# Optimization experiments

Hardware: AMD Instinct MI355X
Metric: run time of the kernel (lower is better)

## Reference

```python
import jax, jax.numpy as jnp
import numpy as np

B, C_IN, C_OUT, H, K = 256, 64, 64, 1855, 6


def setup_inputs() -> dict:
    key = jax.random.key(0)
    k1, k2, k3, k4 = jax.random.split(key, 4)
    x = jax.random.normal(k1, (B, C_IN, H), dtype=jnp.float32)
    # hex-grid neighbor table; -1 marks missing neighbors (camera boundary).
    neighbors = jax.random.randint(k2, (H, K), 0, H, dtype=jnp.int32)
    # row 0 fully valid is not required -- module uses row 0 to compute total_valid.
    mask = jax.random.uniform(k3, (H, K)) < 0.1
    neighbors = jnp.where(mask, -1, neighbors)
    weight_center = jax.random.normal(k4, (C_OUT, C_IN), dtype=jnp.float32) / np.sqrt(C_IN)
    weight_neighbors = jax.random.normal(jax.random.fold_in(key, 5), (C_OUT, C_IN, K), dtype=jnp.float32) / np.sqrt(C_IN * K)
    bias = jnp.zeros((C_OUT,), dtype=jnp.float32)
    return {"x": x, "neighbors": neighbors, "weight_center": weight_center,
            "weight_neighbors": weight_neighbors, "bias": bias}


def reference(x, neighbors, weight_center, weight_neighbors, bias):
    # x: [B, C_in, H] -> [B, H, C_in]
    xt = jnp.swapaxes(x, 1, 2)
    # center contribution: [B, H, C_out]
    center = jnp.einsum('bhc,oc->bho', xt, weight_center)
    valid = neighbors >= 0                      # [H, K]
    idx = jnp.where(valid, neighbors, 0)        # safe gather indices
    nf = xt[:, idx]                             # [B, H, K, C_in] gathered neighbors
    nf = nf * valid[None, :, :, None].astype(xt.dtype)
    neighbor_contrib = jnp.einsum('bhkc,ock->bho', nf, weight_neighbors)
    # module divides by (#valid neighbors of hexagon 0) + 1
    total_valid = (valid[0].sum() + 1).astype(xt.dtype)
    out = (center + neighbor_contrib) / total_valid + bias
    return jnp.swapaxes(out, 1, 2)              # [B, C_out, H]
```

## Files before the change

### kernel.cpp

```cpp
#include <hip/hip_runtime.h>
#include <hip/hip_bf16.h>

#define B_    256
#define CIN   64
#define COUT  64
#define H_    1855
#define K_    6
#define NSTEP 14
#define HT    64
#define NHT   29

#define HT2   32
#define TPB   58
#define NTILE (TPB * B_)
#define TPBLK 8
#define NBLK  (NTILE / TPBLK)
#define CPX2  (NBLK / 8)

typedef __bf16 bf16x8 __attribute__((ext_vector_type(8)));
typedef float  f32x4  __attribute__((ext_vector_type(4)));

typedef __attribute__((address_space(3))) unsigned int       lds_u32;
typedef const __attribute__((address_space(1))) unsigned int glb_u32;

static __device__ inline unsigned short f2bf(float f) {
    __hip_bfloat16 h = __float2bfloat16(f);
    return *reinterpret_cast<unsigned short*>(&h);
}

__global__ void prep_weights(const float* __restrict__ wc,
                             const float* __restrict__ wn,
                             const int*   __restrict__ nb,
                             unsigned short* __restrict__ W2,
                             float* __restrict__ inv_tv,
                             unsigned short* __restrict__ zbuf) {
    int e = blockIdx.x * 256 + threadIdx.x;
    int j = e & 7;
    int l = (e >> 3) & 63;
    int t = (e >> 9) & 3;
    int s = e >> 11;
    int o = t * 16 + (l & 15);
    int k = s * 32 + (l >> 4) * 8 + j;
    int slot = k >> 6;
    int c = k & 63;
    float v = (slot == 0) ? wc[o * 64 + c]
                          : wn[(o * 64 + c) * 6 + (slot - 1)];
    W2[e] = f2bf(v);
    if (blockIdx.x == 0 && threadIdx.x < 64) zbuf[threadIdx.x] = 0;
    if (e == 0) {
        int cnt = 1;
        #pragma unroll
        for (int q = 0; q < 6; ++q) cnt += (nb[q] >= 0) ? 1 : 0;
        *inv_tv = 1.0f / (float)cnt;
    }
}

__global__ void transpose_bf16(const float* __restrict__ x,
                               unsigned short* __restrict__ xT) {
    __shared__ __align__(16) unsigned short tile[64][72];
    int b  = blockIdx.y;
    int h0 = blockIdx.x * HT;
    int t  = threadIdx.x;
    int ho = t & 63;
    int cq = t >> 6;
    const float* xb = x + (size_t)b * CIN * H_;
    int h = h0 + ho;
    #pragma unroll
    for (int i = 0; i < 16; ++i) {
        int c = i * 4 + cq;
        float v = (h < H_) ? xb[(size_t)c * H_ + h] : 0.f;
        tile[ho][c] = f2bf(v);
    }
    __syncthreads();
    #pragma unroll
    for (int rep = 0; rep < 2; ++rep) {
        int task = rep * 256 + t;
        int hh = task >> 3;
        int j  = task & 7;
        int hw = h0 + hh;
        if (hw < H_) {
            *reinterpret_cast<uint4*>(&xT[((size_t)b * H_ + hw) * 64 + j * 8]) =
                *reinterpret_cast<const uint4*>(&tile[hh][j * 8]);
        }
    }
}

__global__ __launch_bounds__(512, 4) void conv_main(
        const unsigned short* __restrict__ xT,
        const unsigned short* __restrict__ W2,
        const int*   __restrict__ nb,
        const float* __restrict__ bias,
        const float* __restrict__ inv_tv,
        const unsigned short* __restrict__ zbuf,
        float* __restrict__ out) {
    __shared__ __align__(16) unsigned short feat[2][6][HT2][64];

    int bid = blockIdx.x;
    int swz   = (bid & 7) * CPX2 + (bid >> 3);
    int gbase = swz * TPBLK;

    int t = threadIdx.x;
    int w = t >> 6;
    int l = t & 63;

    int lrow = l >> 3;
    int jsrc = (l & 7) ^ lrow;
    int qm[3], rq[3];
    #pragma unroll
    for (int c = 0; c < 3; ++c) {
        int m = w * 3 + c;
        qm[c] = m >> 2;
        rq[c] = (m & 3) * 8;
    }

    int og = w & 3, hh = w >> 2;
    int lr = l & 15, lg = l >> 4;
    int hrow = hh * 16 + lr;
    int sw8  = hrow & 7;

    const bf16x8* __restrict__ Wf = reinterpret_cast<const bf16x8*>(W2);
    bf16x8 wr[NSTEP];
    #pragma unroll
    for (int s = 0; s < NSTEP; ++s) wr[s] = Wf[(s * 4 + og) * 64 + l];
    #pragma unroll
    for (int s = 0; s < NSTEP; ++s) asm volatile("" : "+v"(wr[s]));

    float inv = *inv_tv;
    float bv[4];
    #pragma unroll
    for (int r = 0; r < 4; ++r) bv[r] = bias[og * 16 + lg * 4 + r];

    int nbv[2][3];
    bf16x8 cc[2][2];

    {
        int b0  = gbase / TPB;
        int h00 = (gbase - b0 * TPB) * HT2;
        int nb0[3];
        #pragma unroll
        for (int c = 0; c < 3; ++c) {
            int h = h00 + rq[c] + lrow;
            nb0[c] = (h < H_) ? nb[h * 6 + qm[c]] : -1;
        }
        const unsigned short* xb = xT + (size_t)b0 * H_ * 64;
        int hcl = h00 + hrow; if (hcl >= H_) hcl = H_ - 1;
        const bf16x8* crow = reinterpret_cast<const bf16x8*>(xb + (size_t)hcl * 64);
        cc[0][0] = crow[lg];
        cc[0][1] = crow[4 + lg];
        #pragma unroll
        for (int c = 0; c < 3; ++c) {
            int n = nb0[c];
            const unsigned short* src = (n >= 0)
                ? (xb + (size_t)n * 64 + jsrc * 8) : (zbuf + jsrc * 8);
            __builtin_amdgcn_global_load_lds((glb_u32*)src,
                (lds_u32*)&feat[0][qm[c]][rq[c]][0], 16, 0, 0);
        }
        int g1 = gbase + 1;
        int b1 = g1 / TPB;
        int h01 = (g1 - b1 * TPB) * HT2;
        #pragma unroll
        for (int c = 0; c < 3; ++c) {
            int h = h01 + rq[c] + lrow;
            nbv[1][c] = (h < H_) ? nb[h * 6 + qm[c]] : -1;
        }
    }

    #pragma unroll
    for (int i = 0; i < TPBLK; ++i) {
        if (i < TPBLK - 2) {
            int g2 = gbase + i + 2;
            int b2 = g2 / TPB;
            int h02 = (g2 - b2 * TPB) * HT2;
            #pragma unroll
            for (int c = 0; c < 3; ++c) {
                int h = h02 + rq[c] + lrow;
                nbv[i & 1][c] = (h < H_) ? nb[h * 6 + qm[c]] : -1;
            }
        }
        if (i < TPBLK - 1) {
            int g1 = gbase + i + 1;
            int b1 = g1 / TPB;
            int h01 = (g1 - b1 * TPB) * HT2;
            const unsigned short* xb = xT + (size_t)b1 * H_ * 64;
            int nbuf = (i + 1) & 1;
            int hcl = h01 + hrow; if (hcl >= H_) hcl = H_ - 1;
            const bf16x8* crow = reinterpret_cast<const bf16x8*>(xb + (size_t)hcl * 64);
            cc[nbuf][0] = crow[lg];
            cc[nbuf][1] = crow[4 + lg];
            #pragma unroll
            for (int c = 0; c < 3; ++c) {
                int n = nbv[nbuf][c];
                const unsigned short* src = (n >= 0)
                    ? (xb + (size_t)n * 64 + jsrc * 8) : (zbuf + jsrc * 8);
                __builtin_amdgcn_global_load_lds((glb_u32*)src,
                    (lds_u32*)&feat[nbuf][qm[c]][rq[c]][0], 16, 0, 0);
            }
        }
        if (i == TPBLK - 1)
            asm volatile("s_waitcnt vmcnt(4)" ::: "memory");
        else if (i == TPBLK - 2)
            asm volatile("s_waitcnt vmcnt(9)" ::: "memory");
        else
            asm volatile("s_waitcnt vmcnt(12)" ::: "memory");
        __builtin_amdgcn_s_barrier();
        __builtin_amdgcn_sched_barrier(0);

        int cb = i & 1;
        f32x4 acc = (f32x4){0.f, 0.f, 0.f, 0.f};
        acc = __builtin_amdgcn_mfma_f32_16x16x32_bf16(wr[0], cc[cb][0], acc, 0, 0, 0);
        acc = __builtin_amdgcn_mfma_f32_16x16x32_bf16(wr[1], cc[cb][1], acc, 0, 0, 0);
        #pragma unroll
        for (int q = 0; q < 6; ++q) {
            bf16x8 fa = *reinterpret_cast<const bf16x8*>(
                    &feat[cb][q][hrow][(lg ^ sw8) * 8]);
            bf16x8 fb = *reinterpret_cast<const bf16x8*>(
                    &feat[cb][q][hrow][((4 + lg) ^ sw8) * 8]);
            acc = __builtin_amdgcn_mfma_f32_16x16x32_bf16(wr[2 + 2 * q], fa, acc, 0, 0, 0);
            acc = __builtin_amdgcn_mfma_f32_16x16x32_bf16(wr[3 + 2 * q], fb, acc, 0, 0, 0);
        }

        int g    = gbase + i;
        int curb = g / TPB;
        int curh = (g - curb * TPB) * HT2 + hrow;
        if (curh < H_) {
            float* ob = out + (size_t)curb * COUT * H_ + curh;
            #pragma unroll
            for (int r = 0; r < 4; ++r)
                ob[(size_t)(og * 16 + lg * 4 + r) * H_] = acc[r] * inv + bv[r];
        }

        __builtin_amdgcn_s_barrier();
    }
}

extern "C" void kernel_launch(void* const* d_in, const int* in_sizes, int n_in,
                              void* d_out, int out_size, void* d_ws, size_t ws_size,
                              hipStream_t stream) {
    const float* x    = (const float*)d_in[0];
    const int*   nb   = (const int*)  d_in[1];
    const float* wc   = (const float*)d_in[2];
    const float* wn   = (const float*)d_in[3];
    const float* bias = (const float*)d_in[4];
    float* out = (float*)d_out;

    char* ws = (char*)d_ws;
    unsigned short* W2     = (unsigned short*)ws;
    float*          inv_tv = (float*)(ws + 57344);
    unsigned short* zbuf   = (unsigned short*)(ws + 57472);
    unsigned short* xT     = (unsigned short*)(ws + 57600);

    prep_weights<<<112, 256, 0, stream>>>(wc, wn, nb, W2, inv_tv, zbuf);

    dim3 tgrid(NHT, B_);
    transpose_bf16<<<tgrid, 256, 0, stream>>>(x, xT);
    conv_main<<<NBLK, 512, 0, stream>>>(xT, W2, nb, bias, inv_tv, zbuf, out);
}
```

Measured before the change: 128.1 us.

## Shrink conv tiles to 16 hexes, 4 waves, stage center rows via LDS

```diff
diff --git a/kernel.cpp b/kernel.cpp
--- a/kernel.cpp
+++ b/kernel.cpp
@@ -10,12 +10,12 @@
 #define HT    64
 #define NHT   29
 
-#define HT2   32
-#define TPB   58
-#define NTILE (TPB * B_)
-#define TPBLK 8
-#define NBLK  (NTILE / TPBLK)
-#define CPX2  (NBLK / 8)
+#define HT3    16
+#define TPB2   116
+#define NTILE2 (TPB2 * B_)
+#define TPBLK2 16
+#define NBLK3  (NTILE2 / TPBLK2)
+#define CPX4   (NBLK3 / 8)
 
 typedef __bf16 bf16x8 __attribute__((ext_vector_type(8)));
 typedef float  f32x4  __attribute__((ext_vector_type(4)));
@@ -85,7 +85,7 @@
     }
 }
 
-__global__ __launch_bounds__(512, 4) void conv_main(
+__global__ __launch_bounds__(256, 5) void conv_main(
         const unsigned short* __restrict__ xT,
         const unsigned short* __restrict__ W2,
         const int*   __restrict__ nb,
@@ -93,11 +93,11 @@
         const float* __restrict__ inv_tv,
         const unsigned short* __restrict__ zbuf,
         float* __restrict__ out) {
-    __shared__ __align__(16) unsigned short feat[2][6][HT2][64];
+    __shared__ __align__(16) unsigned short feat[2][7][HT3][64];
 
     int bid = blockIdx.x;
-    int swz   = (bid & 7) * CPX2 + (bid >> 3);
-    int gbase = swz * TPBLK;
+    int swz   = (bid & 7) * CPX4 + (bid >> 3);
+    int gbase = swz * TPBLK2;
 
     int t = threadIdx.x;
     int w = t >> 6;
@@ -105,25 +105,24 @@
 
     int lrow = l >> 3;
     int jsrc = (l & 7) ^ lrow;
-    int qm[3], rq[3];
+    int slotc[3], halfc[3], nbq[3];
     #pragma unroll
     for (int c = 0; c < 3; ++c) {
         int m = w * 3 + c;
-        qm[c] = m >> 2;
-        rq[c] = (m & 3) * 8;
-    }
-
-    int og = w & 3, hh = w >> 2;
+        nbq[c]   = m >> 1;
+        slotc[c] = 1 + (m >> 1);
+        halfc[c] = (m & 1) * 8;
+    }
+    bool hasC = (w < 2);
+
+    int og = w;
     int lr = l & 15, lg = l >> 4;
-    int hrow = hh * 16 + lr;
-    int sw8  = hrow & 7;
+    int sw8 = lr & 7;
 
     const bf16x8* __restrict__ Wf = reinterpret_cast<const bf16x8*>(W2);
     bf16x8 wr[NSTEP];
     #pragma unroll
     for (int s = 0; s < NSTEP; ++s) wr[s] = Wf[(s * 4 + og) * 64 + l];
-    #pragma unroll
-    for (int s = 0; s < NSTEP; ++s) asm volatile("" : "+v"(wr[s]));
 
     float inv = *inv_tv;
     float bv[4];
@@ -131,97 +130,105 @@
     for (int r = 0; r < 4; ++r) bv[r] = bias[og * 16 + lg * 4 + r];
 
     int nbv[2][3];
-    bf16x8 cc[2][2];
 
     {
-        int b0  = gbase / TPB;
-        int h00 = (gbase - b0 * TPB) * HT2;
+        int g0  = gbase;
+        int b0  = g0 / TPB2;
+        int h00 = (g0 - b0 * TPB2) * HT3;
         int nb0[3];
         #pragma unroll
         for (int c = 0; c < 3; ++c) {
-            int h = h00 + rq[c] + lrow;
-            nb0[c] = (h < H_) ? nb[h * 6 + qm[c]] : -1;
+            int h = h00 + halfc[c] + lrow;
+            nb0[c] = (h < H_) ? nb[h * 6 + nbq[c]] : -1;
         }
         const unsigned short* xb = xT + (size_t)b0 * H_ * 64;
-        int hcl = h00 + hrow; if (hcl >= H_) hcl = H_ - 1;
-        const bf16x8* crow = reinterpret_cast<const bf16x8*>(xb + (size_t)hcl * 64);
-        cc[0][0] = crow[lg];
-        cc[0][1] = crow[4 + lg];
         #pragma unroll
         for (int c = 0; c < 3; ++c) {
             int n = nb0[c];
             const unsigned short* src = (n >= 0)
                 ? (xb + (size_t)n * 64 + jsrc * 8) : (zbuf + jsrc * 8);
             __builtin_amdgcn_global_load_lds((glb_u32*)src,
-                (lds_u32*)&feat[0][qm[c]][rq[c]][0], 16, 0, 0);
-        }
-        int g1 = gbase + 1;
-        int b1 = g1 / TPB;
-        int h01 = (g1 - b1 * TPB) * HT2;
+                (lds_u32*)&feat[0][slotc[c]][halfc[c]][0], 16, 0, 0);
+        }
+        if (hasC) {
+            int hc = h00 + w * 8 + lrow; if (hc >= H_) hc = H_ - 1;
+            __builtin_amdgcn_global_load_lds(
+                (glb_u32*)(xb + (size_t)hc * 64 + jsrc * 8),
+                (lds_u32*)&feat[0][0][w * 8][0], 16, 0, 0);
+        }
+        int g1  = gbase + 1;
+        int b1  = g1 / TPB2;
+        int h01 = (g1 - b1 * TPB2) * HT3;
         #pragma unroll
         for (int c = 0; c < 3; ++c) {
-            int h = h01 + rq[c] + lrow;
-            nbv[1][c] = (h < H_) ? nb[h * 6 + qm[c]] : -1;
-        }
-    }
-
-    #pragma unroll
-    for (int i = 0; i < TPBLK; ++i) {
-        if (i < TPBLK - 2) {
-            int g2 = gbase + i + 2;
-            int b2 = g2 / TPB;
-            int h02 = (g2 - b2 * TPB) * HT2;
+            int h = h01 + halfc[c] + lrow;
+            nbv[1][c] = (h < H_) ? nb[h * 6 + nbq[c]] : -1;
+        }
+    }
+
+    #pragma unroll
+    for (int i = 0; i < TPBLK2; ++i) {
+        if (i < TPBLK2 - 2) {
+            int g2  = gbase + i + 2;
+            int b2  = g2 / TPB2;
+            int h02 = (g2 - b2 * TPB2) * HT3;
             #pragma unroll
             for (int c = 0; c < 3; ++c) {
-                int h = h02 + rq[c] + lrow;
-                nbv[i & 1][c] = (h < H_) ? nb[h * 6 + qm[c]] : -1;
+                int h = h02 + halfc[c] + lrow;
+                nbv[i & 1][c] = (h < H_) ? nb[h * 6 + nbq[c]] : -1;
             }
         }
-        if (i < TPBLK - 1) {
-            int g1 = gbase + i + 1;
-            int b1 = g1 / TPB;
-            int h01 = (g1 - b1 * TPB) * HT2;
+        if (i < TPBLK2 - 1) {
+            int g1  = gbase + i + 1;
+            int b1  = g1 / TPB2;
+            int h01 = (g1 - b1 * TPB2) * HT3;
             const unsigned short* xb = xT + (size_t)b1 * H_ * 64;
             int nbuf = (i + 1) & 1;
-            int hcl = h01 + hrow; if (hcl >= H_) hcl = H_ - 1;
-            const bf16x8* crow = reinterpret_cast<const bf16x8*>(xb + (size_t)hcl * 64);
-            cc[nbuf][0] = crow[lg];
-            cc[nbuf][1] = crow[4 + lg];
             #pragma unroll
             for (int c = 0; c < 3; ++c) {
                 int n = nbv[nbuf][c];
                 const unsigned short* src = (n >= 0)
                     ? (xb + (size_t)n * 64 + jsrc * 8) : (zbuf + jsrc * 8);
                 __builtin_amdgcn_global_load_lds((glb_u32*)src,
-                    (lds_u32*)&feat[nbuf][qm[c]][rq[c]][0], 16, 0, 0);
+                    (lds_u32*)&feat[nbuf][slotc[c]][halfc[c]][0], 16, 0, 0);
             }
-        }
-        if (i == TPBLK - 1)
+            if (hasC) {
+                int hc = h01 + w * 8 + lrow; if (hc >= H_) hc = H_ - 1;
+                __builtin_amdgcn_global_load_lds(
+                    (glb_u32*)(xb + (size_t)hc * 64 + jsrc * 8),
+                    (lds_u32*)&feat[nbuf][0][w * 8][0], 16, 0, 0);
+            }
+        }
+        if (i == TPBLK2 - 1) {
             asm volatile("s_waitcnt vmcnt(4)" ::: "memory");
-        else if (i == TPBLK - 2)
-            asm volatile("s_waitcnt vmcnt(9)" ::: "memory");
-        else
-            asm volatile("s_waitcnt vmcnt(12)" ::: "memory");
+        } else if (i == TPBLK2 - 2) {
+            if (hasC) asm volatile("s_waitcnt vmcnt(8)" ::: "memory");
+            else      asm volatile("s_waitcnt vmcnt(7)" ::: "memory");
+        } else if (i == 0) {
+            if (hasC) asm volatile("s_waitcnt vmcnt(10)" ::: "memory");
+            else      asm volatile("s_waitcnt vmcnt(9)" ::: "memory");
+        } else {
+            if (hasC) asm volatile("s_waitcnt vmcnt(11)" ::: "memory");
+            else      asm volatile("s_waitcnt vmcnt(10)" ::: "memory");
+        }
         __builtin_amdgcn_s_barrier();
         __builtin_amdgcn_sched_barrier(0);
 
         int cb = i & 1;
         f32x4 acc = (f32x4){0.f, 0.f, 0.f, 0.f};
-        acc = __builtin_amdgcn_mfma_f32_16x16x32_bf16(wr[0], cc[cb][0], acc, 0, 0, 0);
-        acc = __builtin_amdgcn_mfma_f32_16x16x32_bf16(wr[1], cc[cb][1], acc, 0, 0, 0);
-        #pragma unroll
-        for (int q = 0; q < 6; ++q) {
+        #pragma unroll
+        for (int s = 0; s < 7; ++s) {
             bf16x8 fa = *reinterpret_cast<const bf16x8*>(
-                    &feat[cb][q][hrow][(lg ^ sw8) * 8]);
+                    &feat[cb][s][lr][(lg ^ sw8) * 8]);
             bf16x8 fb = *reinterpret_cast<const bf16x8*>(
-                    &feat[cb][q][hrow][((4 + lg) ^ sw8) * 8]);
-            acc = __builtin_amdgcn_mfma_f32_16x16x32_bf16(wr[2 + 2 * q], fa, acc, 0, 0, 0);
-            acc = __builtin_amdgcn_mfma_f32_16x16x32_bf16(wr[3 + 2 * q], fb, acc, 0, 0, 0);
+                    &feat[cb][s][lr][((4 + lg) ^ sw8) * 8]);
+            acc = __builtin_amdgcn_mfma_f32_16x16x32_bf16(wr[2 * s],     fa, acc, 0, 0, 0);
+            acc = __builtin_amdgcn_mfma_f32_16x16x32_bf16(wr[2 * s + 1], fb, acc, 0, 0, 0);
         }
 
         int g    = gbase + i;
-        int curb = g / TPB;
-        int curh = (g - curb * TPB) * HT2 + hrow;
+        int curb = g / TPB2;
+        int curh = (g - curb * TPB2) * HT3 + lr;
         if (curh < H_) {
             float* ob = out + (size_t)curb * COUT * H_ + curh;
             #pragma unroll
@@ -253,5 +260,5 @@
 
     dim3 tgrid(NHT, B_);
     transpose_bf16<<<tgrid, 256, 0, stream>>>(x, xT);
-    conv_main<<<NBLK, 512, 0, stream>>>(xT, W2, nb, bias, inv_tv, zbuf, out);
-}
+    conv_main<<<NBLK3, 256, 0, stream>>>(xT, W2, nb, bias, inv_tv, zbuf, out);
+}
```

After: 175.8 us. +37.3%, slower.
